# Performance work log

Hardware: AMD Instinct MI355X
Metric: run time of the kernel (lower is better)

## Reference

```python
import jax, jax.numpy as jnp
import numpy as np

N = 100000
E = 1600000
D_IN = 64
D_HID = 64
D_OUT = 64
R = 8
BN_EPS = 1e-5


def setup_inputs() -> dict:
    key = jax.random.key(0)
    ks = jax.random.split(key, 12)
    x = jax.random.normal(ks[0], (N, D_IN), dtype=jnp.float32)
    edge_index = jax.random.randint(ks[1], (2, E), 0, N, dtype=jnp.int64)
    edge_type = jax.random.randint(ks[2], (E,), 0, R, dtype=jnp.int64)
    s1 = 1.0 / np.sqrt(D_IN)
    s2 = 1.0 / np.sqrt(D_HID)
    w1 = jax.random.uniform(ks[3], (R, D_IN, D_HID), jnp.float32, -s1, s1)
    root1 = jax.random.uniform(ks[4], (D_IN, D_HID), jnp.float32, -s1, s1)
    b1 = jnp.zeros((D_HID,), jnp.float32)
    gamma1 = jnp.ones((D_HID,), jnp.float32)
    beta1 = jnp.zeros((D_HID,), jnp.float32)
    w2 = jax.random.uniform(ks[5], (R, D_HID, D_OUT), jnp.float32, -s2, s2)
    root2 = jax.random.uniform(ks[6], (D_HID, D_OUT), jnp.float32, -s2, s2)
    b2 = jnp.zeros((D_OUT,), jnp.float32)
    return {"x": x, "edge_index": edge_index, "edge_type": edge_type,
            "w1": w1, "root1": root1, "b1": b1, "gamma1": gamma1, "beta1": beta1,
            "w2": w2, "root2": root2, "b2": b2}


def rgcn_conv(x, edge_index, edge_type, W, root, bias):
    # PyG RGCNConv with aggr='mean': per relation r, mean of neighbor features
    # over incoming edges of type r, transformed by W[r]; plus root transform + bias.
    # Aggregate-then-transform (legal since transform is linear): one fused
    # segment_sum keyed by (dst, relation), then a grouped GEMM via einsum.
    n, d = x.shape
    src, dst = edge_index[0], edge_index[1]
    seg = dst * R + edge_type                     # [E] combined segment id
    msg = x[src]                                  # [E, d] gather
    agg = jax.ops.segment_sum(msg, seg, num_segments=n * R).reshape(n, R, d)
    cnt = jax.ops.segment_sum(jnp.ones((src.shape[0],), x.dtype), seg,
                              num_segments=n * R).reshape(n, R, 1)
    mean = agg / jnp.maximum(cnt, 1.0)            # [n, R, d]
    return jnp.einsum('nrd,rdo->no', mean, W) + x @ root + bias


def batch_norm(h, gamma, beta):
    mu = h.mean(axis=0)
    var = h.var(axis=0)
    return gamma * (h - mu) * jax.lax.rsqrt(var + BN_EPS) + beta


def reference(x, edge_index, edge_type, w1, root1, b1, gamma1, beta1, w2, root2, b2):
    h = rgcn_conv(x, edge_index, edge_type, w1, root1, b1)
    h = jax.nn.relu(batch_norm(h, gamma1, beta1))
    # dropout: identity (eval mode)
    out = rgcn_conv(h, edge_index, edge_type, w2, root2, b2)
    return out
```

## Files before the change

### kernel.cpp

```cpp
#include <hip/hip_runtime.h>
#include <hip/hip_bf16.h>

#define NN 100000
#define EE 1600000
#define RR 8
#define DD 64
#define MM (NN * RR)
#define BN_EPS 1e-5f
#define KTOT 576
#define BSTRIDE 584

#define NB 391
#define EPB 8192
#define NBIN ((EE + EPB - 1) / EPB)

typedef __bf16 bf16x8 __attribute__((ext_vector_type(8)));
typedef float  f32x4  __attribute__((ext_vector_type(4)));

static __device__ __forceinline__ unsigned short f32_to_bf16(float f) {
    unsigned int u = __float_as_uint(f);
    unsigned int r = u + 0x7FFFu + ((u >> 16) & 1u);
    return (unsigned short)(r >> 16);
}
static __device__ __forceinline__ float bflo(unsigned int u) {
    return __uint_as_float(u << 16);
}
static __device__ __forceinline__ float bfhi(unsigned int u) {
    return __uint_as_float(u & 0xFFFF0000u);
}


__global__ void k_bcount(const int* __restrict__ dst, int* __restrict__ btot) {
    __shared__ int cnt[NB];
    int t = threadIdx.x;
    for (int i = t; i < NB; i += 256) cnt[i] = 0;
    __syncthreads();
    int base = blockIdx.x * EPB;
#pragma unroll
    for (int i = 0; i < EPB / 256; ++i) {
        int e = base + i * 256 + t;
        if (e < EE) atomicAdd(&cnt[dst[e] >> 8], 1);
    }
    __syncthreads();
    for (int i = t; i < NB; i += 256)
        if (cnt[i]) atomicAdd(&btot[i], cnt[i]);
}

__global__ void k_bscan(const int* __restrict__ btot, int* __restrict__ bbase,
                        int* __restrict__ gcur, int* __restrict__ rowptr) {
    __shared__ int sd[512];
    int t = threadIdx.x;
    int v = (t < NB) ? btot[t] : 0;
    sd[t] = v;
    __syncthreads();
    for (int off = 1; off < 512; off <<= 1) {
        int x = (t >= off) ? sd[t - off] : 0;
        __syncthreads();
        sd[t] += x;
        __syncthreads();
    }
    if (t < NB) { bbase[t] = sd[t] - v; gcur[t] = sd[t] - v; }
    if (t == NB - 1) { bbase[NB] = sd[t]; rowptr[MM] = sd[t]; }
}

__global__ void k_bin(const int* __restrict__ src, const int* __restrict__ dst,
                      const int* __restrict__ et, int* __restrict__ gcur,
                      unsigned int* __restrict__ ebuf) {
    __shared__ int cnt[NB];
    __shared__ int bas[NB];
    __shared__ int off[NB];
    int t = threadIdx.x;
    for (int i = t; i < NB; i += 256) { cnt[i] = 0; off[i] = 0; }
    __syncthreads();
    int base = blockIdx.x * EPB;
#pragma unroll
    for (int i = 0; i < EPB / 256; ++i) {
        int e = base + i * 256 + t;
        if (e < EE) atomicAdd(&cnt[dst[e] >> 8], 1);
    }
    __syncthreads();
    for (int i = t; i < NB; i += 256) {
        int c = cnt[i];
        bas[i] = c ? atomicAdd(&gcur[i], c) : 0;
    }
    __syncthreads();
#pragma unroll
    for (int i = 0; i < EPB / 256; ++i) {
        int e = base + i * 256 + t;
        if (e < EE) {
            int d = dst[e];
            int b = d >> 8;
            int lk = ((d & 255) << 3) | et[e];
            unsigned int rec0 = (unsigned int)src[e] | ((unsigned int)lk << 17);
            int p = bas[b] + atomicAdd(&off[b], 1);
            ebuf[p] = rec0;
        }
    }
}

__global__ __launch_bounds__(256) void k_bcsr(const int* __restrict__ bbase,
                                              const unsigned int* __restrict__ ebuf,
                                              int* __restrict__ rowptr,
                                              int* __restrict__ rec) {
    __shared__ int deg[2048];
    __shared__ int part[256];
    int b = blockIdx.x, t = threadIdx.x;
    int e0 = bbase[b], e1 = bbase[b + 1];
    for (int i = t; i < 2048; i += 256) deg[i] = 0;
    __syncthreads();
    for (int e = e0 + t; e < e1; e += 256) atomicAdd(&deg[ebuf[e] >> 17], 1);
    __syncthreads();
    int loc[8];
    int s = 0;
#pragma unroll
    for (int j = 0; j < 8; ++j) { loc[j] = deg[t * 8 + j]; s += loc[j]; }
    part[t] = s;
    __syncthreads();
    for (int off = 1; off < 256; off <<= 1) {
        int x = (t >= off) ? part[t - off] : 0;
        __syncthreads();
        part[t] += x;
        __syncthreads();
    }
    int run = part[t] - s;
    int keyBase = b * 2048;
#pragma unroll
    for (int j = 0; j < 8; ++j) {
        int g = keyBase + t * 8 + j;
        if (g < MM) rowptr[g] = e0 + run;
        deg[t * 8 + j] = run;
        run += loc[j];
    }
    __syncthreads();
    for (int e = e0 + t; e < e1; e += 256) {
        unsigned int v = ebuf[e];
        int lk = v >> 17;
        int pos = e0 + atomicAdd(&deg[lk], 1);
        rec[pos] = (int)(v & 0x1FFFFu);
    }
}


__global__ void k_tobf16(const float* __restrict__ X, unsigned short* __restrict__ Xb) {
    int i = blockIdx.x * 256 + threadIdx.x;
    if (i >= NN * DD / 4) return;
    float4 v = ((const float4*)X)[i];
    ushort4 o;
    o.x = f32_to_bf16(v.x); o.y = f32_to_bf16(v.y);
    o.z = f32_to_bf16(v.z); o.w = f32_to_bf16(v.w);
    ((ushort4*)Xb)[i] = o;
}


__global__ void k_prepw(const float* __restrict__ W, const float* __restrict__ Root,
                        unsigned short* __restrict__ WcT) {
    int i = blockIdx.x * 256 + threadIdx.x;
    if (i >= 64 * KTOT) return;
    int o = i / KTOT;
    int k = i - o * KTOT;
    float v;
    if (k < 512) v = W[(size_t)(k >> 6) * 4096 + (k & 63) * 64 + o];
    else         v = Root[(k - 512) * 64 + o];
    WcT[(size_t)o * KTOT + k] = f32_to_bf16(v);
}


__global__ __launch_bounds__(256, 8) void k_fused(const unsigned short* __restrict__ Xb,
                                                  const int* __restrict__ rowptr,
                                                  const int* __restrict__ rec,
                                                  const unsigned short* __restrict__ WcT,
                                                  const float* __restrict__ bias,
                                                  float* __restrict__ Out,
                                                  float* __restrict__ stats,
                                                  int dostats) {
    __shared__ unsigned short Atile[16 * BSTRIDE];
    int t = threadIdx.x;
    int wv = t >> 6, lane = t & 63;
    int r = lane >> 3;
    int q = lane & 7;
    int nodeBase = blockIdx.x * 16;
    int wnode = nodeBase + wv * 4;
    int v0 = rowptr[wnode * RR + (lane < 33 ? lane : 32)];

    if (lane < 32) {
        int i = lane >> 3, c = lane & 7;
        uint4 xv = *(const uint4*)(Xb + (size_t)(wnode + i) * DD + c * 8);
        *(uint4*)(Atile + (size_t)(wv * 4 + i) * BSTRIDE + 512 + c * 8) = xv;
    }

#pragma unroll 1
    for (int i = 0; i < 4; ++i) {
        int e0 = __shfl(v0, i * 8 + r);
        int e1 = __shfl(v0, i * 8 + r + 1);
        float a0[8] = {0,0,0,0,0,0,0,0};
        float a1[8] = {0,0,0,0,0,0,0,0};
        float a2[8] = {0,0,0,0,0,0,0,0};
        float a3[8] = {0,0,0,0,0,0,0,0};
        int e = e0;
        for (; e + 3 < e1; e += 4) {
            int s0 = rec[e], s1 = rec[e + 1], s2 = rec[e + 2], s3 = rec[e + 3];
            uint4 u0 = *(const uint4*)(Xb + (size_t)s0 * DD + q * 8);
            uint4 u1 = *(const uint4*)(Xb + (size_t)s1 * DD + q * 8);
            uint4 u2 = *(const uint4*)(Xb + (size_t)s2 * DD + q * 8);
            uint4 u3 = *(const uint4*)(Xb + (size_t)s3 * DD + q * 8);
            a0[0] += bflo(u0.x); a0[1] += bfhi(u0.x); a0[2] += bflo(u0.y); a0[3] += bfhi(u0.y);
            a0[4] += bflo(u0.z); a0[5] += bfhi(u0.z); a0[6] += bflo(u0.w); a0[7] += bfhi(u0.w);
            a1[0] += bflo(u1.x); a1[1] += bfhi(u1.x); a1[2] += bflo(u1.y); a1[3] += bfhi(u1.y);
            a1[4] += bflo(u1.z); a1[5] += bfhi(u1.z); a1[6] += bflo(u1.w); a1[7] += bfhi(u1.w);
            a2[0] += bflo(u2.x); a2[1] += bfhi(u2.x); a2[2] += bflo(u2.y); a2[3] += bfhi(u2.y);
            a2[4] += bflo(u2.z); a2[5] += bfhi(u2.z); a2[6] += bflo(u2.w); a2[7] += bfhi(u2.w);
            a3[0] += bflo(u3.x); a3[1] += bfhi(u3.x); a3[2] += bflo(u3.y); a3[3] += bfhi(u3.y);
            a3[4] += bflo(u3.z); a3[5] += bfhi(u3.z); a3[6] += bflo(u3.w); a3[7] += bfhi(u3.w);
        }
        if (e + 1 < e1) {
            int s0 = rec[e], s1 = rec[e + 1];
            uint4 u0 = *(const uint4*)(Xb + (size_t)s0 * DD + q * 8);
            uint4 u1 = *(const uint4*)(Xb + (size_t)s1 * DD + q * 8);
            a0[0] += bflo(u0.x); a0[1] += bfhi(u0.x); a0[2] += bflo(u0.y); a0[3] += bfhi(u0.y);
            a0[4] += bflo(u0.z); a0[5] += bfhi(u0.z); a0[6] += bflo(u0.w); a0[7] += bfhi(u0.w);
            a1[0] += bflo(u1.x); a1[1] += bfhi(u1.x); a1[2] += bflo(u1.y); a1[3] += bfhi(u1.y);
            a1[4] += bflo(u1.z); a1[5] += bfhi(u1.z); a1[6] += bflo(u1.w); a1[7] += bfhi(u1.w);
            e += 2;
        }
        if (e < e1) {
            int s0 = rec[e];
            uint4 u0 = *(const uint4*)(Xb + (size_t)s0 * DD + q * 8);
            a0[0] += bflo(u0.x); a0[1] += bfhi(u0.x); a0[2] += bflo(u0.y); a0[3] += bfhi(u0.y);
            a0[4] += bflo(u0.z); a0[5] += bfhi(u0.z); a0[6] += bflo(u0.w); a0[7] += bfhi(u0.w);
        }
        int cnt = e1 - e0;
        float inv = 1.0f / (float)(cnt > 1 ? cnt : 1);
        uint4 o;
        o.x = (unsigned)f32_to_bf16((a0[0]+a1[0]+a2[0]+a3[0]) * inv) | ((unsigned)f32_to_bf16((a0[1]+a1[1]+a2[1]+a3[1]) * inv) << 16);
        o.y = (unsigned)f32_to_bf16((a0[2]+a1[2]+a2[2]+a3[2]) * inv) | ((unsigned)f32_to_bf16((a0[3]+a1[3]+a2[3]+a3[3]) * inv) << 16);
        o.z = (unsigned)f32_to_bf16((a0[4]+a1[4]+a2[4]+a3[4]) * inv) | ((unsigned)f32_to_bf16((a0[5]+a1[5]+a2[5]+a3[5]) * inv) << 16);
        o.w = (unsigned)f32_to_bf16((a0[6]+a1[6]+a2[6]+a3[6]) * inv) | ((unsigned)f32_to_bf16((a0[7]+a1[7]+a2[7]+a3[7]) * inv) << 16);
        *(uint4*)(Atile + (size_t)(wv * 4 + i) * BSTRIDE + lane * 8) = o;
    }
    __syncthreads();

    int m16 = lane & 15, quad = lane >> 4;
    const unsigned short* as = Atile + m16 * BSTRIDE + quad * 8;
    const unsigned short* bg = WcT + (size_t)(wv * 16 + m16) * KTOT + quad * 8;
    union AU { uint4 u; bf16x8 f; };
    f32x4 acc = (f32x4){0.f, 0.f, 0.f, 0.f};
#pragma unroll
    for (int kb = 0; kb < 18; ++kb) {
        AU av, bv;
        av.u = *(const uint4*)(as + kb * 32);
        bv.u = *(const uint4*)(bg + kb * 32);
        acc = __builtin_amdgcn_mfma_f32_16x16x32_bf16(av.f, bv.f, acc, 0, 0, 0);
    }

    int row0 = nodeBase + quad * 4;
    int col = wv * 16 + m16;
    float bb = bias[col];
    float s = 0.f, sq = 0.f;
#pragma unroll
    for (int i2 = 0; i2 < 4; ++i2) {
        float v = acc[i2] + bb;
        Out[(size_t)(row0 + i2) * 64 + col] = v;
        s += v; sq += v * v;
    }
    if (dostats) {
        s += __shfl_xor(s, 16); s += __shfl_xor(s, 32);
        sq += __shfl_xor(sq, 16); sq += __shfl_xor(sq, 32);
        if (quad == 0) {
            atomicAdd(&stats[col], s);
            atomicAdd(&stats[64 + col], sq);
        }
    }
}


__global__ void k_bnrelu(const float* __restrict__ H, unsigned short* __restrict__ Hb,
                         const float* __restrict__ stats,
                         const float* __restrict__ gamma, const float* __restrict__ beta) {
    int idx = blockIdx.x * 256 + threadIdx.x;
    const int total = NN * DD / 4;
    if (idx >= total) return;
    int c0 = (idx & 15) * 4;
    float4 v = ((const float4*)H)[idx];
    float inv = 1.0f / (float)NN;
    float4 o;
    {
        float mu = stats[c0 + 0] * inv;
        float var = stats[64 + c0 + 0] * inv - mu * mu;
        float sc = gamma[c0 + 0] * rsqrtf(var + BN_EPS);
        float r = sc * (v.x - mu) + beta[c0 + 0];
        o.x = r > 0.f ? r : 0.f;
    }
    {
        float mu = stats[c0 + 1] * inv;
        float var = stats[64 + c0 + 1] * inv - mu * mu;
        float sc = gamma[c0 + 1] * rsqrtf(var + BN_EPS);
        float r = sc * (v.y - mu) + beta[c0 + 1];
        o.y = r > 0.f ? r : 0.f;
    }
    {
        float mu = stats[c0 + 2] * inv;
        float var = stats[64 + c0 + 2] * inv - mu * mu;
        float sc = gamma[c0 + 2] * rsqrtf(var + BN_EPS);
        float r = sc * (v.z - mu) + beta[c0 + 2];
        o.z = r > 0.f ? r : 0.f;
    }
    {
        float mu = stats[c0 + 3] * inv;
        float var = stats[64 + c0 + 3] * inv - mu * mu;
        float sc = gamma[c0 + 3] * rsqrtf(var + BN_EPS);
        float r = sc * (v.w - mu) + beta[c0 + 3];
        o.w = r > 0.f ? r : 0.f;
    }
    ushort4 ob;
    ob.x = f32_to_bf16(o.x); ob.y = f32_to_bf16(o.y);
    ob.z = f32_to_bf16(o.z); ob.w = f32_to_bf16(o.w);
    ((ushort4*)Hb)[idx] = ob;
}


static inline size_t alignup(size_t x) { return (x + 255) & ~(size_t)255; }

extern "C" void kernel_launch(void* const* d_in, const int* in_sizes, int n_in,
                              void* d_out, int out_size, void* d_ws, size_t ws_size,
                              hipStream_t stream) {
    const float* x      = (const float*)d_in[0];
    const int*   eidx   = (const int*)d_in[1];
    const int*   etype  = (const int*)d_in[2];
    const float* w1     = (const float*)d_in[3];
    const float* root1  = (const float*)d_in[4];
    const float* b1     = (const float*)d_in[5];
    const float* gamma1 = (const float*)d_in[6];
    const float* beta1  = (const float*)d_in[7];
    const float* w2     = (const float*)d_in[8];
    const float* root2  = (const float*)d_in[9];
    const float* b2     = (const float*)d_in[10];
    float* out = (float*)d_out;

    const int* src = eidx;
    const int* dst = eidx + EE;

    char* w = (char*)d_ws;
    int* rowptr = (int*)w;            w += alignup((size_t)(MM + 1) * 4);
    int* btot   = (int*)w;            w += alignup(512 * 4);
    int* bbase  = (int*)w;            w += alignup(512 * 4);
    int* gcur   = (int*)w;            w += alignup(512 * 4);
    int* rec    = (int*)w;            w += alignup((size_t)EE * 4);
    float* h    = (float*)w;          w += alignup((size_t)NN * DD * 4);
    unsigned short* xhb = (unsigned short*)w; w += alignup((size_t)NN * DD * 2);
    unsigned short* wct1 = (unsigned short*)w; w += alignup((size_t)64 * KTOT * 2);
    unsigned short* wct2 = (unsigned short*)w; w += alignup((size_t)64 * KTOT * 2);
    float* stats = (float*)w;         w += alignup(128 * 4);
    unsigned int* ebuf = (unsigned int*)h;

    hipMemsetAsync(btot, 0, 512 * 4, stream);
    hipMemsetAsync(stats, 0, 128 * 4, stream);

    k_prepw<<<dim3(144), dim3(256), 0, stream>>>(w1, root1, wct1);
    k_prepw<<<dim3(144), dim3(256), 0, stream>>>(w2, root2, wct2);
    k_tobf16<<<dim3(NN * DD / 4 / 256 + 1), dim3(256), 0, stream>>>(x, xhb);

    k_bcount<<<dim3(NBIN), dim3(256), 0, stream>>>(dst, btot);
    k_bscan<<<dim3(1), dim3(512), 0, stream>>>(btot, bbase, gcur, rowptr);
    k_bin<<<dim3(NBIN), dim3(256), 0, stream>>>(src, dst, etype, gcur, ebuf);
    k_bcsr<<<dim3(NB), dim3(256), 0, stream>>>(bbase, ebuf, rowptr, rec);

    k_fused<<<dim3(NN / 16), dim3(256), 0, stream>>>(xhb, rowptr, rec, wct1, b1, h, stats, 1);
    k_bnrelu<<<dim3(NN * DD / 4 / 256), dim3(256), 0, stream>>>(h, xhb, stats, gamma1, beta1);

    k_fused<<<dim3(NN / 16), dim3(256), 0, stream>>>(xhb, rowptr, rec, wct2, b2, out, stats, 0);
}
```

Measured before the change: 452.6 us.

## Use 16 waves per block: one node per wave, split-K MFMA with LDS reduction

The fused gather+GEMM kernel now launches 1024 threads per block, so each wave aggregates one node instead of looping over four, which adds memory-level parallelism for the gather. The 18 MFMA k-steps are split across four wave groups (split-K), and partial accumulators are combined through an LDS buffer before bias, store and stats. This trades an extra barrier, LDS traffic and idle waves in the epilogue for more concurrent gather loads and shorter per-wave latency chains.

```diff
diff --git a/kernel.cpp b/kernel.cpp
--- a/kernel.cpp
+++ b/kernel.cpp
@@ -165,109 +165,112 @@
 }
 
 
-__global__ __launch_bounds__(256, 8) void k_fused(const unsigned short* __restrict__ Xb,
-                                                  const int* __restrict__ rowptr,
-                                                  const int* __restrict__ rec,
-                                                  const unsigned short* __restrict__ WcT,
-                                                  const float* __restrict__ bias,
-                                                  float* __restrict__ Out,
-                                                  float* __restrict__ stats,
-                                                  int dostats) {
+__global__ __launch_bounds__(1024, 4) void k_fused(const unsigned short* __restrict__ Xb,
+                                                   const int* __restrict__ rowptr,
+                                                   const int* __restrict__ rec,
+                                                   const unsigned short* __restrict__ WcT,
+                                                   const float* __restrict__ bias,
+                                                   float* __restrict__ Out,
+                                                   float* __restrict__ stats,
+                                                   int dostats) {
     __shared__ unsigned short Atile[16 * BSTRIDE];
+    __shared__ f32x4 pbuf[12][64];
     int t = threadIdx.x;
     int wv = t >> 6, lane = t & 63;
     int r = lane >> 3;
     int q = lane & 7;
     int nodeBase = blockIdx.x * 16;
-    int wnode = nodeBase + wv * 4;
-    int v0 = rowptr[wnode * RR + (lane < 33 ? lane : 32)];
-
-    if (lane < 32) {
-        int i = lane >> 3, c = lane & 7;
-        uint4 xv = *(const uint4*)(Xb + (size_t)(wnode + i) * DD + c * 8);
-        *(uint4*)(Atile + (size_t)(wv * 4 + i) * BSTRIDE + 512 + c * 8) = xv;
-    }
-
-#pragma unroll 1
-    for (int i = 0; i < 4; ++i) {
-        int e0 = __shfl(v0, i * 8 + r);
-        int e1 = __shfl(v0, i * 8 + r + 1);
-        float a0[8] = {0,0,0,0,0,0,0,0};
-        float a1[8] = {0,0,0,0,0,0,0,0};
-        float a2[8] = {0,0,0,0,0,0,0,0};
-        float a3[8] = {0,0,0,0,0,0,0,0};
-        int e = e0;
-        for (; e + 3 < e1; e += 4) {
-            int s0 = rec[e], s1 = rec[e + 1], s2 = rec[e + 2], s3 = rec[e + 3];
-            uint4 u0 = *(const uint4*)(Xb + (size_t)s0 * DD + q * 8);
-            uint4 u1 = *(const uint4*)(Xb + (size_t)s1 * DD + q * 8);
-            uint4 u2 = *(const uint4*)(Xb + (size_t)s2 * DD + q * 8);
-            uint4 u3 = *(const uint4*)(Xb + (size_t)s3 * DD + q * 8);
-            a0[0] += bflo(u0.x); a0[1] += bfhi(u0.x); a0[2] += bflo(u0.y); a0[3] += bfhi(u0.y);
-            a0[4] += bflo(u0.z); a0[5] += bfhi(u0.z); a0[6] += bflo(u0.w); a0[7] += bfhi(u0.w);
-            a1[0] += bflo(u1.x); a1[1] += bfhi(u1.x); a1[2] += bflo(u1.y); a1[3] += bfhi(u1.y);
-            a1[4] += bflo(u1.z); a1[5] += bfhi(u1.z); a1[6] += bflo(u1.w); a1[7] += bfhi(u1.w);
-            a2[0] += bflo(u2.x); a2[1] += bfhi(u2.x); a2[2] += bflo(u2.y); a2[3] += bfhi(u2.y);
-            a2[4] += bflo(u2.z); a2[5] += bfhi(u2.z); a2[6] += bflo(u2.w); a2[7] += bfhi(u2.w);
-            a3[0] += bflo(u3.x); a3[1] += bfhi(u3.x); a3[2] += bflo(u3.y); a3[3] += bfhi(u3.y);
-            a3[4] += bflo(u3.z); a3[5] += bfhi(u3.z); a3[6] += bflo(u3.w); a3[7] += bfhi(u3.w);
-        }
-        if (e + 1 < e1) {
-            int s0 = rec[e], s1 = rec[e + 1];
-            uint4 u0 = *(const uint4*)(Xb + (size_t)s0 * DD + q * 8);
-            uint4 u1 = *(const uint4*)(Xb + (size_t)s1 * DD + q * 8);
-            a0[0] += bflo(u0.x); a0[1] += bfhi(u0.x); a0[2] += bflo(u0.y); a0[3] += bfhi(u0.y);
-            a0[4] += bflo(u0.z); a0[5] += bfhi(u0.z); a0[6] += bflo(u0.w); a0[7] += bfhi(u0.w);
-            a1[0] += bflo(u1.x); a1[1] += bfhi(u1.x); a1[2] += bflo(u1.y); a1[3] += bfhi(u1.y);
-            a1[4] += bflo(u1.z); a1[5] += bfhi(u1.z); a1[6] += bflo(u1.w); a1[7] += bfhi(u1.w);
-            e += 2;
-        }
-        if (e < e1) {
-            int s0 = rec[e];
-            uint4 u0 = *(const uint4*)(Xb + (size_t)s0 * DD + q * 8);
-            a0[0] += bflo(u0.x); a0[1] += bfhi(u0.x); a0[2] += bflo(u0.y); a0[3] += bfhi(u0.y);
-            a0[4] += bflo(u0.z); a0[5] += bfhi(u0.z); a0[6] += bflo(u0.w); a0[7] += bfhi(u0.w);
-        }
-        int cnt = e1 - e0;
-        float inv = 1.0f / (float)(cnt > 1 ? cnt : 1);
-        uint4 o;
-        o.x = (unsigned)f32_to_bf16((a0[0]+a1[0]+a2[0]+a3[0]) * inv) | ((unsigned)f32_to_bf16((a0[1]+a1[1]+a2[1]+a3[1]) * inv) << 16);
-        o.y = (unsigned)f32_to_bf16((a0[2]+a1[2]+a2[2]+a3[2]) * inv) | ((unsigned)f32_to_bf16((a0[3]+a1[3]+a2[3]+a3[3]) * inv) << 16);
-        o.z = (unsigned)f32_to_bf16((a0[4]+a1[4]+a2[4]+a3[4]) * inv) | ((unsigned)f32_to_bf16((a0[5]+a1[5]+a2[5]+a3[5]) * inv) << 16);
-        o.w = (unsigned)f32_to_bf16((a0[6]+a1[6]+a2[6]+a3[6]) * inv) | ((unsigned)f32_to_bf16((a0[7]+a1[7]+a2[7]+a3[7]) * inv) << 16);
-        *(uint4*)(Atile + (size_t)(wv * 4 + i) * BSTRIDE + lane * 8) = o;
-    }
+    int n = nodeBase + wv;
+    int v0 = rowptr[n * RR + (lane < 9 ? lane : 8)];
+    int e0 = __shfl(v0, r);
+    int e1 = __shfl(v0, r + 1);
+
+    if (lane < 8) {
+        uint4 xv = *(const uint4*)(Xb + (size_t)n * DD + lane * 8);
+        *(uint4*)(Atile + (size_t)wv * BSTRIDE + 512 + lane * 8) = xv;
+    }
+
+    float a[8] = {0,0,0,0,0,0,0,0};
+    int e = e0;
+    for (; e + 3 < e1; e += 4) {
+        int s0 = rec[e], s1 = rec[e + 1], s2 = rec[e + 2], s3 = rec[e + 3];
+        uint4 u0 = *(const uint4*)(Xb + (size_t)s0 * DD + q * 8);
+        uint4 u1 = *(const uint4*)(Xb + (size_t)s1 * DD + q * 8);
+        uint4 u2 = *(const uint4*)(Xb + (size_t)s2 * DD + q * 8);
+        uint4 u3 = *(const uint4*)(Xb + (size_t)s3 * DD + q * 8);
+        a[0] += bflo(u0.x); a[1] += bfhi(u0.x); a[2] += bflo(u0.y); a[3] += bfhi(u0.y);
+        a[4] += bflo(u0.z); a[5] += bfhi(u0.z); a[6] += bflo(u0.w); a[7] += bfhi(u0.w);
+        a[0] += bflo(u1.x); a[1] += bfhi(u1.x); a[2] += bflo(u1.y); a[3] += bfhi(u1.y);
+        a[4] += bflo(u1.z); a[5] += bfhi(u1.z); a[6] += bflo(u1.w); a[7] += bfhi(u1.w);
+        a[0] += bflo(u2.x); a[1] += bfhi(u2.x); a[2] += bflo(u2.y); a[3] += bfhi(u2.y);
+        a[4] += bflo(u2.z); a[5] += bfhi(u2.z); a[6] += bflo(u2.w); a[7] += bfhi(u2.w);
+        a[0] += bflo(u3.x); a[1] += bfhi(u3.x); a[2] += bflo(u3.y); a[3] += bfhi(u3.y);
+        a[4] += bflo(u3.z); a[5] += bfhi(u3.z); a[6] += bflo(u3.w); a[7] += bfhi(u3.w);
+    }
+    if (e + 1 < e1) {
+        int s0 = rec[e], s1 = rec[e + 1];
+        uint4 u0 = *(const uint4*)(Xb + (size_t)s0 * DD + q * 8);
+        uint4 u1 = *(const uint4*)(Xb + (size_t)s1 * DD + q * 8);
+        a[0] += bflo(u0.x); a[1] += bfhi(u0.x); a[2] += bflo(u0.y); a[3] += bfhi(u0.y);
+        a[4] += bflo(u0.z); a[5] += bfhi(u0.z); a[6] += bflo(u0.w); a[7] += bfhi(u0.w);
+        a[0] += bflo(u1.x); a[1] += bfhi(u1.x); a[2] += bflo(u1.y); a[3] += bfhi(u1.y);
+        a[4] += bflo(u1.z); a[5] += bfhi(u1.z); a[6] += bflo(u1.w); a[7] += bfhi(u1.w);
+        e += 2;
+    }
+    if (e < e1) {
+        int s0 = rec[e];
+        uint4 u0 = *(const uint4*)(Xb + (size_t)s0 * DD + q * 8);
+        a[0] += bflo(u0.x); a[1] += bfhi(u0.x); a[2] += bflo(u0.y); a[3] += bfhi(u0.y);
+        a[4] += bflo(u0.z); a[5] += bfhi(u0.z); a[6] += bflo(u0.w); a[7] += bfhi(u0.w);
+    }
+    int cnt = e1 - e0;
+    float inv = 1.0f / (float)(cnt > 1 ? cnt : 1);
+    uint4 o;
+    o.x = (unsigned)f32_to_bf16(a[0] * inv) | ((unsigned)f32_to_bf16(a[1] * inv) << 16);
+    o.y = (unsigned)f32_to_bf16(a[2] * inv) | ((unsigned)f32_to_bf16(a[3] * inv) << 16);
+    o.z = (unsigned)f32_to_bf16(a[4] * inv) | ((unsigned)f32_to_bf16(a[5] * inv) << 16);
+    o.w = (unsigned)f32_to_bf16(a[6] * inv) | ((unsigned)f32_to_bf16(a[7] * inv) << 16);
+    *(uint4*)(Atile + (size_t)wv * BSTRIDE + lane * 8) = o;
     __syncthreads();
 
     int m16 = lane & 15, quad = lane >> 4;
+    int c = wv & 3, s = wv >> 2;
+    int kb0 = s * 4 + (s < 2 ? s : 2);
+    int kcnt = (s < 2) ? 5 : 4;
     const unsigned short* as = Atile + m16 * BSTRIDE + quad * 8;
-    const unsigned short* bg = WcT + (size_t)(wv * 16 + m16) * KTOT + quad * 8;
+    const unsigned short* bg = WcT + (size_t)(c * 16 + m16) * KTOT + quad * 8;
     union AU { uint4 u; bf16x8 f; };
     f32x4 acc = (f32x4){0.f, 0.f, 0.f, 0.f};
-#pragma unroll
-    for (int kb = 0; kb < 18; ++kb) {
+    for (int kb = kb0; kb < kb0 + kcnt; ++kb) {
         AU av, bv;
         av.u = *(const uint4*)(as + kb * 32);
         bv.u = *(const uint4*)(bg + kb * 32);
         acc = __builtin_amdgcn_mfma_f32_16x16x32_bf16(av.f, bv.f, acc, 0, 0, 0);
     }
-
-    int row0 = nodeBase + quad * 4;
-    int col = wv * 16 + m16;
-    float bb = bias[col];
-    float s = 0.f, sq = 0.f;
-#pragma unroll
-    for (int i2 = 0; i2 < 4; ++i2) {
-        float v = acc[i2] + bb;
-        Out[(size_t)(row0 + i2) * 64 + col] = v;
-        s += v; sq += v * v;
-    }
-    if (dostats) {
-        s += __shfl_xor(s, 16); s += __shfl_xor(s, 32);
-        sq += __shfl_xor(sq, 16); sq += __shfl_xor(sq, 32);
-        if (quad == 0) {
-            atomicAdd(&stats[col], s);
-            atomicAdd(&stats[64 + col], sq);
+    if (s) pbuf[(s - 1) * 4 + c][lane] = acc;
+    __syncthreads();
+    if (s == 0) {
+        f32x4 p0 = pbuf[c][lane];
+        f32x4 p1 = pbuf[4 + c][lane];
+        f32x4 p2 = pbuf[8 + c][lane];
+        acc = acc + p0 + p1 + p2;
+        int row0 = nodeBase + quad * 4;
+        int col = c * 16 + m16;
+        float bb = bias[col];
+        float sm = 0.f, sq = 0.f;
+#pragma unroll
+        for (int i2 = 0; i2 < 4; ++i2) {
+            float v = acc[i2] + bb;
+            Out[(size_t)(row0 + i2) * 64 + col] = v;
+            sm += v; sq += v * v;
+        }
+        if (dostats) {
+            sm += __shfl_xor(sm, 16); sm += __shfl_xor(sm, 32);
+            sq += __shfl_xor(sq, 16); sq += __shfl_xor(sq, 32);
+            if (quad == 0) {
+                atomicAdd(&stats[col], sm);
+                atomicAdd(&stats[64 + col], sq);
+            }
         }
     }
 }
@@ -364,8 +367,8 @@
     k_bin<<<dim3(NBIN), dim3(256), 0, stream>>>(src, dst, etype, gcur, ebuf);
     k_bcsr<<<dim3(NB), dim3(256), 0, stream>>>(bbase, ebuf, rowptr, rec);
 
-    k_fused<<<dim3(NN / 16), dim3(256), 0, stream>>>(xhb, rowptr, rec, wct1, b1, h, stats, 1);
+    k_fused<<<dim3(NN / 16), dim3(1024), 0, stream>>>(xhb, rowptr, rec, wct1, b1, h, stats, 1);
     k_bnrelu<<<dim3(NN * DD / 4 / 256), dim3(256), 0, stream>>>(h, xhb, stats, gamma1, beta1);
 
-    k_fused<<<dim3(NN / 16), dim3(256), 0, stream>>>(xhb, rowptr, rec, wct2, b2, out, stats, 0);
-}
+    k_fused<<<dim3(NN / 16), dim3(1024), 0, stream>>>(xhb, rowptr, rec, wct2, b2, out, stats, 0);
+}
```

Result: no change. 453.2 us (+0.1%).
